# Optimization experiments

Hardware: AMD Instinct MI355X
Metric: run time of the kernel (lower is better)

The kernel has to match this reference:

```python
import jax, jax.numpy as jnp
import numpy as np

B = 16          # events per minibatch
P = 4096        # generated points per event
Q = 4096        # ground-truth points per event
SPATIAL_SIZE = 256.0


def setup_inputs() -> dict:
    key = jax.random.key(0)
    k1, k2 = jax.random.split(key)
    points_gen = jax.random.normal(k1, (B * P, 3), dtype=jnp.float32)
    # batch ids: contiguous equal-size segments per event
    batch_gen = (jnp.arange(B * P, dtype=jnp.int32) // P).astype(jnp.int32)
    # label: col 0 = batch id, cols 1:4 = coords in [0, 256), col 4 = class label
    coords = jax.random.uniform(k2, (B * Q, 3), dtype=jnp.float32) * SPATIAL_SIZE
    batch_gt = (jnp.arange(B * Q, dtype=jnp.float32) // Q)
    cls = jnp.zeros((B * Q,), dtype=jnp.float32)
    label = jnp.concatenate([batch_gt[:, None], coords, cls[:, None]], axis=1)
    return {"points_gen": points_gen, "batch_gen": batch_gen, "label": label}


def _chamfer(x, y):
    # x: [P,3], y: [Q,3] -> symmetric Chamfer distance (squared Euclidean)
    x2 = jnp.sum(x * x, axis=-1)                      # [P]
    y2 = jnp.sum(y * y, axis=-1)                      # [Q]
    d = x2[:, None] + y2[None, :] - 2.0 * (x @ y.T)   # [P,Q]
    return jnp.mean(jnp.min(d, axis=1)) + jnp.mean(jnp.min(d, axis=0))


def reference(points_gen, batch_gen, label):
    half = SPATIAL_SIZE / 2.0
    points_gt = (label[:, 1:4] - half) / half          # normalize GT to [-1,1]
    # batch ids are contiguous equal segments -> masking == reshape
    x = points_gen.reshape(B, P, 3)
    y = points_gt.reshape(B, Q, 3)
    losses = jax.vmap(_chamfer)(x, y)                  # [B]
    loss = jnp.sum(losses) / B                         # loss / count
    return loss
```

## Files before the change

kernel.cpp:

```cpp
#include <hip/hip_runtime.h>


#define NB 16
#define NP 4096
#define THREADS 256
#define INV128 0.0078125f
#define FINF __int_as_float(0x7F800000)

typedef __attribute__((ext_vector_type(8)))  short bf16x8;
typedef __attribute__((ext_vector_type(16))) float f32x16;

__device__ __forceinline__ short bf16rne(float f) {
    unsigned u = __float_as_uint(f);
    return (short)((u + 0x7FFFu + ((u >> 16) & 1u)) >> 16);
}
__device__ __forceinline__ float bf2f(short s) {
    return __uint_as_float(((unsigned)(unsigned short)s) << 16);
}

__global__ __launch_bounds__(THREADS) void chamfer_kernel(const float* __restrict__ gen,
                                                          const float* __restrict__ label,
                                                          float* __restrict__ partial) {
    __shared__ short spack[NP * 8 + 1280];
    __shared__ float wpart[8];

    const int bid   = blockIdx.x;
    const int dir   = bid >> 8;
    const int b     = (bid >> 4) & 15;
    const int qpair = bid & 15;
    const int tid   = threadIdx.x;
    const int lane  = tid & 63;
    const int wave  = tid >> 6;
    const int base  = b * NP;

    if (tid < 8) spack[NP * 8 + tid] = 0;

    #pragma unroll 4
    for (int k = 0; k < 16; ++k) {
        int j = tid + k * 256;
        float x, y, z;
        if (dir == 0) {
            const float* row = label + (size_t)(base + j) * 5;
            x = fmaf(row[1], INV128, -1.0f);
            y = fmaf(row[2], INV128, -1.0f);
            z = fmaf(row[3], INV128, -1.0f);
        } else {
            const float* g = gen + (size_t)(base + j) * 3;
            x = g[0]; y = g[1]; z = g[2];
        }
        float t2 = fmaf(x, x, fmaf(y, y, z * z));
        short xh = bf16rne(x), yh = bf16rne(y), zh = bf16rne(z);
        short xl = bf16rne(x - bf2f(xh));
        short yl = bf16rne(y - bf2f(yh));
        short zl = bf16rne(z - bf2f(zh));
        short th = bf16rne(t2);
        short tl = bf16rne(t2 - bf2f(th));
        bf16x8 v = {xh, yh, zh, xl, yl, zl, th, tl};
        *(bf16x8*)(spack + j * 8) = v;
    }
    __syncthreads();

    float sacc = 0.0f;
    const f32x16 zc = {};

    #pragma unroll 1
    for (int sub = 0; sub < 2; ++sub) {
        const int qblk = qpair * 2 + sub;

        const int qrow = base + qblk * 128 + wave * 32 + (lane & 31);
        float q2 = 0.0f;
        bf16x8 afrag = (bf16x8)(short)0;
        if (lane < 32) {
            float x, y, z;
            if (dir == 0) {
                const float* g = gen + (size_t)qrow * 3;
                x = g[0]; y = g[1]; z = g[2];
            } else {
                const float* row = label + (size_t)qrow * 5;
                x = fmaf(row[1], INV128, -1.0f);
                y = fmaf(row[2], INV128, -1.0f);
                z = fmaf(row[3], INV128, -1.0f);
            }
            q2 = fmaf(x, x, fmaf(y, y, z * z));
            short ax = bf16rne(-2.0f * x), ay = bf16rne(-2.0f * y), az = bf16rne(-2.0f * z);
            const short one = 0x3F80;
            bf16x8 a = {ax, ay, az, ax, ay, az, one, one};
            afrag = a;
        }

        float mn[16];
        #pragma unroll
        for (int r = 0; r < 16; ++r) mn[r] = FINF;

        const short* zl = spack + NP * 8;
        const short* p0 = (lane < 32) ? (spack + (lane & 31) * 8)       : zl;
        const short* p1 = (lane < 32) ? (spack + (lane & 31) * 8 + 256) : zl;
        const short* p2 = (lane < 32) ? (spack + (lane & 31) * 8 + 512) : zl;
        const short* p3 = (lane < 32) ? (spack + (lane & 31) * 8 + 768) : zl;
        const int step = (lane < 32) ? 1024 : 0;

        bf16x8 b0 = *(const bf16x8*)p0;
        bf16x8 b1 = *(const bf16x8*)p1;
        bf16x8 b2 = *(const bf16x8*)p2;
        bf16x8 b3 = *(const bf16x8*)p3;
        #pragma unroll 2
        for (int it = 0; it < 32; ++it) {
            p0 += step; p1 += step; p2 += step; p3 += step;
            bf16x8 n0 = *(const bf16x8*)p0;
            bf16x8 n1 = *(const bf16x8*)p1;
            bf16x8 n2 = *(const bf16x8*)p2;
            bf16x8 n3 = *(const bf16x8*)p3;
            f32x16 c0 = __builtin_amdgcn_mfma_f32_32x32x16_bf16(afrag, b0, zc, 0, 0, 0);
            f32x16 c1 = __builtin_amdgcn_mfma_f32_32x32x16_bf16(afrag, b1, zc, 0, 0, 0);
            f32x16 c2 = __builtin_amdgcn_mfma_f32_32x32x16_bf16(afrag, b2, zc, 0, 0, 0);
            f32x16 c3 = __builtin_amdgcn_mfma_f32_32x32x16_bf16(afrag, b3, zc, 0, 0, 0);
            #pragma unroll
            for (int r = 0; r < 16; ++r) {
                mn[r] = fminf(fminf(c0[r], c1[r]),
                              fminf(fminf(c2[r], c3[r]), mn[r]));
            }
            b0 = n0; b1 = n1; b2 = n2; b3 = n3;
        }

        #pragma unroll
        for (int m = 1; m <= 16; m <<= 1) {
            #pragma unroll
            for (int r = 0; r < 16; ++r)
                mn[r] = fminf(mn[r], __shfl_xor(mn[r], m, 64));
        }

        const int h4 = (lane >> 5) * 4;
        #pragma unroll
        for (int r = 0; r < 16; ++r) {
            int row = (r & 3) + 8 * (r >> 2) + h4;
            sacc += mn[r] + __shfl(q2, row, 64);
        }
    }

    if ((lane & 31) == 0) wpart[wave * 2 + (lane >> 5)] = sacc;
    __syncthreads();
    if (tid == 0) {
        float t = 0.0f;
        #pragma unroll
        for (int i = 0; i < 8; ++i) t += wpart[i];
        partial[bid] = t;
    }
}

__global__ __launch_bounds__(256) void reduce_kernel(const float* __restrict__ partial,
                                                     float* __restrict__ out) {
    int i = threadIdx.x;
    float s = partial[i] + partial[i + 256];
    #pragma unroll
    for (int off = 32; off > 0; off >>= 1) s += __shfl_down(s, off, 64);
    __shared__ float ws4[4];
    if ((i & 63) == 0) ws4[i >> 6] = s;
    __syncthreads();
    if (i == 0) out[0] = ((ws4[0] + ws4[1]) + (ws4[2] + ws4[3])) * (1.0f / 65536.0f);
}

extern "C" void kernel_launch(void* const* d_in, const int* in_sizes, int n_in,
                              void* d_out, int out_size, void* d_ws, size_t ws_size,
                              hipStream_t stream) {
    const float* gen   = (const float*)d_in[0];
    const float* label = (const float*)d_in[2];
    float* partial = (float*)d_ws;
    float* out = (float*)d_out;

    chamfer_kernel<<<512, THREADS, 0, stream>>>(gen, label, partial);
    reduce_kernel<<<1, 256, 0, stream>>>(partial, out);
}
```

Before: 91.63 us.

## Split target points across two blocks and merge row minima in a new pass

Each block now scans only half of the target point set (2048 instead of 4096), doubling the grid to 1024 blocks. Per-row minima are written to a global workspace, and a new kernel takes the min of the two halves and sums them before the final reduction. This is meant to give more parallelism and better occupancy on the many CUs and to halve LDS use per block. The cost is one extra launch plus a global write and read of row minima, and each block still reloads its query fragments.

```diff
diff --git a/kernel.cpp b/kernel.cpp
--- a/kernel.cpp
+++ b/kernel.cpp
@@ -3,7 +3,9 @@
 
 #define NB 16
 #define NP 4096
+#define NT 2048
 #define THREADS 256
+#define NROWS 131072
 #define INV128 0.0078125f
 #define FINF __int_as_float(0x7F800000)
 
@@ -20,54 +22,52 @@
 
 __global__ __launch_bounds__(THREADS) void chamfer_kernel(const float* __restrict__ gen,
                                                           const float* __restrict__ label,
-                                                          float* __restrict__ partial) {
-    __shared__ short spack[NP * 8 + 1280];
-    __shared__ float wpart[8];
+                                                          float* __restrict__ rowmins) {
+    __shared__ short spack[NT * 8 + 1280];
 
     const int bid   = blockIdx.x;
-    const int dir   = bid >> 8;
-    const int b     = (bid >> 4) & 15;
-    const int qpair = bid & 15;
+    const int dir   = bid >> 9;
+    const int b     = (bid >> 5) & 15;
+    const int qpair = (bid >> 1) & 15;
+    const int thalf = bid & 1;
     const int tid   = threadIdx.x;
     const int lane  = tid & 63;
     const int wave  = tid >> 6;
     const int base  = b * NP;
+    const int tbase = base + thalf * NT;
 
-    if (tid < 8) spack[NP * 8 + tid] = 0;
+    if (tid < 8) spack[NT * 8 + tid] = 0;
 
     #pragma unroll 4
-    for (int k = 0; k < 16; ++k) {
+    for (int k = 0; k < 8; ++k) {
         int j = tid + k * 256;
         float x, y, z;
         if (dir == 0) {
-            const float* row = label + (size_t)(base + j) * 5;
+            const float* row = label + (size_t)(tbase + j) * 5;
             x = fmaf(row[1], INV128, -1.0f);
             y = fmaf(row[2], INV128, -1.0f);
             z = fmaf(row[3], INV128, -1.0f);
         } else {
-            const float* g = gen + (size_t)(base + j) * 3;
+            const float* g = gen + (size_t)(tbase + j) * 3;
             x = g[0]; y = g[1]; z = g[2];
         }
         float t2 = fmaf(x, x, fmaf(y, y, z * z));
         short xh = bf16rne(x), yh = bf16rne(y), zh = bf16rne(z);
         short xl = bf16rne(x - bf2f(xh));
         short yl = bf16rne(y - bf2f(yh));
-        short zl = bf16rne(z - bf2f(zh));
+        short zl2 = bf16rne(z - bf2f(zh));
         short th = bf16rne(t2);
         short tl = bf16rne(t2 - bf2f(th));
-        bf16x8 v = {xh, yh, zh, xl, yl, zl, th, tl};
+        bf16x8 v = {xh, yh, zh, xl, yl, zl2, th, tl};
         *(bf16x8*)(spack + j * 8) = v;
     }
     __syncthreads();
 
-    float sacc = 0.0f;
     const f32x16 zc = {};
 
     #pragma unroll 1
     for (int sub = 0; sub < 2; ++sub) {
-        const int qblk = qpair * 2 + sub;
-
-        const int qrow = base + qblk * 128 + wave * 32 + (lane & 31);
+        const int qrow = base + qpair * 256 + sub * 128 + wave * 32 + (lane & 31);
         float q2 = 0.0f;
         bf16x8 afrag = (bf16x8)(short)0;
         if (lane < 32) {
@@ -92,7 +92,7 @@
         #pragma unroll
         for (int r = 0; r < 16; ++r) mn[r] = FINF;
 
-        const short* zl = spack + NP * 8;
+        const short* zl = spack + NT * 8;
         const short* p0 = (lane < 32) ? (spack + (lane & 31) * 8)       : zl;
         const short* p1 = (lane < 32) ? (spack + (lane & 31) * 8 + 256) : zl;
         const short* p2 = (lane < 32) ? (spack + (lane & 31) * 8 + 512) : zl;
@@ -104,7 +104,7 @@
         bf16x8 b2 = *(const bf16x8*)p2;
         bf16x8 b3 = *(const bf16x8*)p3;
         #pragma unroll 2
-        for (int it = 0; it < 32; ++it) {
+        for (int it = 0; it < 16; ++it) {
             p0 += step; p1 += step; p2 += step; p3 += step;
             bf16x8 n0 = *(const bf16x8*)p0;
             bf16x8 n1 = *(const bf16x8*)p1;
@@ -130,21 +130,32 @@
         }
 
         const int h4 = (lane >> 5) * 4;
+        const int c  = lane & 31;
+        const int row = (c & 3) + 8 * (c >> 2) + h4;
+        float q2r = __shfl(q2, row & 31, 64);
+        float v = mn[0];
         #pragma unroll
-        for (int r = 0; r < 16; ++r) {
-            int row = (r & 3) + 8 * (r >> 2) + h4;
-            sacc += mn[r] + __shfl(q2, row, 64);
+        for (int r = 1; r < 16; ++r) if (c == r) v = mn[r];
+        if (c < 16) {
+            size_t gidx = (size_t)thalf * NROWS
+                        + (size_t)(((dir * NB + b) << 12) + qpair * 256 + sub * 128
+                                   + wave * 32 + row);
+            rowmins[gidx] = v + q2r;
         }
     }
+}
 
-    if ((lane & 31) == 0) wpart[wave * 2 + (lane >> 5)] = sacc;
+__global__ __launch_bounds__(256) void minsum_kernel(const float* __restrict__ rowmins,
+                                                     float* __restrict__ partial2) {
+    const int tid = threadIdx.x;
+    const int row = blockIdx.x * 256 + tid;
+    float s = fminf(rowmins[row], rowmins[NROWS + row]);
+    #pragma unroll
+    for (int off = 32; off > 0; off >>= 1) s += __shfl_down(s, off, 64);
+    __shared__ float w4[4];
+    if ((tid & 63) == 0) w4[tid >> 6] = s;
     __syncthreads();
-    if (tid == 0) {
-        float t = 0.0f;
-        #pragma unroll
-        for (int i = 0; i < 8; ++i) t += wpart[i];
-        partial[bid] = t;
-    }
+    if (tid == 0) partial2[blockIdx.x] = ((w4[0] + w4[1]) + (w4[2] + w4[3]));
 }
 
 __global__ __launch_bounds__(256) void reduce_kernel(const float* __restrict__ partial,
@@ -164,9 +175,11 @@
                               hipStream_t stream) {
     const float* gen   = (const float*)d_in[0];
     const float* label = (const float*)d_in[2];
-    float* partial = (float*)d_ws;
+    float* rowmins  = (float*)d_ws;
+    float* partial2 = rowmins + 2 * NROWS;
     float* out = (float*)d_out;
 
-    chamfer_kernel<<<512, THREADS, 0, stream>>>(gen, label, partial);
-    reduce_kernel<<<1, 256, 0, stream>>>(partial, out);
+    chamfer_kernel<<<1024, THREADS, 0, stream>>>(gen, label, rowmins);
+    minsum_kernel<<<512, 256, 0, stream>>>(rowmins, partial2);
+    reduce_kernel<<<1, 256, 0, stream>>>(partial2, out);
 }
```

After: 93.88 us. +2.5%, slower.
